# Optimization experiments

Measured on AMD Instinct MI355X. Metric: run time of the kernel, lower is better.

## Reference

```python
import jax, jax.numpy as jnp
import numpy as np

NUM_USERS = 50000
NUM_ITEMS = 10000
NUM_SUPPORT = 5
INPUT_DIM = 512
OUTPUT_DIM = 500
NNZ = 400000


def setup_inputs() -> dict:
    key = jax.random.key(0)
    ks = jax.random.split(key, 6)
    x_u = jax.random.normal(ks[0], (NUM_USERS, INPUT_DIM), dtype=jnp.float32)
    x_v = jax.random.normal(ks[1], (NUM_ITEMS, INPUT_DIM), dtype=jnp.float32)
    # random-uniform-like weight init (weight_variable_random_uniform)
    weights_u = jax.random.normal(ks[2], (INPUT_DIM, OUTPUT_DIM), dtype=jnp.float32) * 0.05
    sup_vals = jax.random.uniform(ks[3], (NUM_SUPPORT, NNZ), dtype=jnp.float32)
    sup_rows = jax.random.randint(ks[4], (NUM_SUPPORT, NNZ), 0, NUM_USERS, dtype=jnp.int32)
    sup_cols = jax.random.randint(ks[5], (NUM_SUPPORT, NNZ), 0, NUM_ITEMS, dtype=jnp.int32)
    return {"x_u": x_u, "x_v": x_v, "weights_u": weights_u,
            "sup_vals": sup_vals, "sup_rows": sup_rows, "sup_cols": sup_cols}


def reference(x_u, x_v, weights_u, sup_vals, sup_rows, sup_cols):
    # share_user_item_weights=True -> weights_v is weights_u; dropout=0.0 -> identity.
    hidden = OUTPUT_DIM // NUM_SUPPORT  # 100
    supports_u, supports_v = [], []
    for i in range(NUM_SUPPORT):
        Wi = jax.lax.dynamic_slice_in_dim(weights_u, i * hidden, hidden, axis=1)
        tmp_u = x_u @ Wi  # [num_users, hidden]
        tmp_v = x_v @ Wi  # [num_items, hidden]
        vals = sup_vals[i][:, None]  # [nnz, 1]
        rows, cols = sup_rows[i], sup_cols[i]
        # support_i @ tmp_v  (sparse [U,I] times dense [I,h])
        su = jax.ops.segment_sum(vals * tmp_v[cols], rows, num_segments=NUM_USERS)
        # support_i^T @ tmp_u (sparse [I,U] times dense [U,h])
        sv = jax.ops.segment_sum(vals * tmp_u[rows], cols, num_segments=NUM_ITEMS)
        supports_u.append(su)
        supports_v.append(sv)
    z_u = jnp.concatenate(supports_u, axis=1)  # [num_users, output_dim]
    z_v = jnp.concatenate(supports_v, axis=1)  # [num_items, output_dim]
    return (jax.nn.relu(z_u), jax.nn.relu(z_v))
```

## Files before the change

### kernel.cpp

```cpp
#include <hip/hip_runtime.h>

#define NUM_USERS   50000
#define NUM_ITEMS   10000
#define NUM_SUPPORT 5
#define INPUT_DIM   512
#define OUTPUT_DIM  500
#define NPAD        512
#define HIDDEN      100
#define HPAD        128
#define NNZ         400000
#define NEDGE       (NUM_SUPPORT * NNZ)

#define CH_E        8192
#define NCHUNK      ((NEDGE + CH_E - 1) / CH_E)
#define NB_U        ((NUM_SUPPORT * NUM_USERS + 255) / 256)
#define NB_V        ((NUM_SUPPORT * NUM_ITEMS + 255) / 256)
#define HISTM_MAX   240000

typedef unsigned int u32;
typedef unsigned short ushort_t;
typedef __attribute__((ext_vector_type(4))) float f32x4;
typedef __attribute__((ext_vector_type(8))) short bf16x8;

#define GLDS(g, l) __builtin_amdgcn_global_load_lds( \
    (const __attribute__((address_space(1))) unsigned int*)(g), \
    (__attribute__((address_space(3))) unsigned int*)(l), 16, 0, 0)

__device__ inline ushort_t bf16_rne(float f) {
    u32 u = __float_as_uint(f);
    u32 r = (u + 0x7FFFu + ((u >> 16) & 1u)) >> 16;
    return (ushort_t)r;
}
__device__ inline float bf16_lo_f32(u32 w) { return __uint_as_float(w << 16); }
__device__ inline float bf16_hi_f32(u32 w) { return __uint_as_float(w & 0xFFFF0000u); }

__global__ __launch_bounds__(256) void cvt_bf16(
    const float4* __restrict__ in, ushort4* __restrict__ out, int n4)
{
    int t = blockIdx.x * 256 + threadIdx.x;
    if (t >= n4) return;
    float4 v = in[t];
    ushort4 o;
    o.x = bf16_rne(v.x); o.y = bf16_rne(v.y);
    o.z = bf16_rne(v.z); o.w = bf16_rne(v.w);
    out[t] = o;
}

__global__ __launch_bounds__(256) void make_WbT(
    const float* __restrict__ W, ushort_t* __restrict__ WbT)
{
    int t = blockIdx.x * 256 + threadIdx.x;
    int n = t >> 9, k = t & 511;
    float v = (n < OUTPUT_DIM) ? W[k * OUTPUT_DIM + n] : 0.f;
    WbT[t] = bf16_rne(v);
}

#define BM 128
#define BN 128
#define BK 32

__global__ __launch_bounds__(256) void gemm_mfma_bf16(
    const ushort_t* __restrict__ A,
    const ushort_t* __restrict__ BT,
    ushort_t* __restrict__ Xp,
    int M)
{
    const int K = INPUT_DIM;
    __shared__ ushort_t As[BM * BK];
    __shared__ ushort_t Bs[BN * BK];

    const int tid  = threadIdx.x;
    const int wave = tid >> 6;
    const int lane = tid & 63;
    const int quad = lane >> 4;
    const int lr   = lane & 15;
    const int m0 = blockIdx.x * BM;
    const int n0 = blockIdx.y * BN;
    const int wm = (wave >> 1) * 64;
    const int wn = (wave & 1) * 64;

    f32x4 acc[4][4] = {};

    for (int k0 = 0; k0 < K; k0 += BK) {
        #pragma unroll
        for (int h = 0; h < 2; ++h) {
            int o   = tid * 16 + h * 4096;
            int row = o >> 6;
            int byt = o & 63;
            int gr  = m0 + row; if (gr >= M) gr = M - 1;
            GLDS((const char*)A + ((long long)gr * K + k0) * 2 + byt, (char*)As + o);
        }
        #pragma unroll
        for (int h = 0; h < 2; ++h) {
            int o   = tid * 16 + h * 4096;
            int row = o >> 6;
            int byt = o & 63;
            GLDS((const char*)BT + ((long long)(n0 + row) * K + k0) * 2 + byt, (char*)Bs + o);
        }
        asm volatile("s_waitcnt vmcnt(0)" ::: "memory");
        __syncthreads();

        bf16x8 af[4], bfr[4];
        #pragma unroll
        for (int tm = 0; tm < 4; ++tm)
            af[tm] = *(const bf16x8*)(As + (wm + tm * 16 + lr) * BK + quad * 8);
        #pragma unroll
        for (int tn = 0; tn < 4; ++tn)
            bfr[tn] = *(const bf16x8*)(Bs + (wn + tn * 16 + lr) * BK + quad * 8);
        #pragma unroll
        for (int tm = 0; tm < 4; ++tm)
            #pragma unroll
            for (int tn = 0; tn < 4; ++tn)
                acc[tm][tn] = __builtin_amdgcn_mfma_f32_16x16x32_bf16(
                    af[tm], bfr[tn], acc[tm][tn], 0, 0, 0);
        __syncthreads();
    }

    #pragma unroll
    for (int tm = 0; tm < 4; ++tm) {
        int rbase = m0 + wm + tm * 16 + quad * 4;
        #pragma unroll
        for (int tn = 0; tn < 4; ++tn) {
            int col = n0 + wn + tn * 16 + lr;
            if (col >= OUTPUT_DIM) continue;
            int seg = col / HIDDEN;
            int off = col - seg * HIDDEN;
            ushort_t* dst = Xp + (long long)seg * M * HPAD + off;
            #pragma unroll
            for (int g = 0; g < 4; ++g) {
                int row = rbase + g;
                if (row < M) dst[(long long)row * HPAD] = bf16_rne(acc[tm][tn][g]);
            }
        }
    }
}

__global__ __launch_bounds__(256) void scan1(u32* __restrict__ data, int n,
                                             u32* __restrict__ partials)
{
    __shared__ u32 sh[256];
    int t = threadIdx.x;
    int base = blockIdx.x * 1024 + t * 4;
    u32 x[4];
    #pragma unroll
    for (int k = 0; k < 4; ++k) {
        int idx = base + k;
        x[k] = (idx < n) ? data[idx] : 0u;
    }
    u32 tsum = x[0] + x[1] + x[2] + x[3];
    sh[t] = tsum;
    __syncthreads();
    for (int off = 1; off < 256; off <<= 1) {
        u32 v = (t >= off) ? sh[t - off] : 0u;
        __syncthreads();
        sh[t] += v;
        __syncthreads();
    }
    u32 run = (t > 0) ? sh[t - 1] : 0u;
    if (t == 255) partials[blockIdx.x] = sh[255];
    #pragma unroll
    for (int k = 0; k < 4; ++k) {
        int idx = base + k;
        if (idx < n) data[idx] = run;
        run += x[k];
    }
}

__global__ __launch_bounds__(256) void scan_partials(u32* __restrict__ partials, int n)
{
    __shared__ u32 sh[256];
    int t = threadIdx.x;
    u32 x = (t < n) ? partials[t] : 0u;
    sh[t] = x;
    __syncthreads();
    for (int off = 1; off < 256; off <<= 1) {
        u32 v = (t >= off) ? sh[t - off] : 0u;
        __syncthreads();
        sh[t] += v;
        __syncthreads();
    }
    if (t < n) partials[t] = (t > 0) ? sh[t - 1] : 0u;
}

__global__ __launch_bounds__(256) void scan_add(u32* __restrict__ data, int n,
                                                const u32* __restrict__ partials)
{
    int idx = blockIdx.x * 256 + threadIdx.x;
    if (idx < n) data[idx] += partials[idx >> 10];
}

template<int NROWS>
__global__ __launch_bounds__(256) void chunk_hist(
    const int* __restrict__ keyidx, u32* __restrict__ histm)
{
    constexpr int NKEY = NUM_SUPPORT * NROWS;
    constexpr int NB = (NKEY + 255) / 256;
    __shared__ u32 hist[NB];
    const int tid = threadIdx.x;
    const int c = blockIdx.x;
    for (int b = tid; b < NB; b += 256) hist[b] = 0u;
    __syncthreads();
    int base = c * CH_E;
    int end = base + CH_E; if (end > NEDGE) end = NEDGE;
    for (int e = base + tid; e < end; e += 256) {
        unsigned i = (unsigned)e / (unsigned)NNZ;
        u32 key = i * (u32)NROWS + (u32)keyidx[e];
        atomicAdd(&hist[key >> 8], 1u);
    }
    __syncthreads();
    for (int b = tid; b < NB; b += 256) histm[b * NCHUNK + c] = hist[b];
}

template<int NROWS, int GSHIFT>
__global__ __launch_bounds__(256) void partition_edges(
    const int* __restrict__ keyidx, const int* __restrict__ gidx,
    const float* __restrict__ vals,
    const u32* __restrict__ histm, uint2* __restrict__ buf)
{
    constexpr int NKEY = NUM_SUPPORT * NROWS;
    constexpr int NB = (NKEY + 255) / 256;
    __shared__ u32 cur[NB];
    const int tid = threadIdx.x;
    const int c = blockIdx.x;
    for (int b = tid; b < NB; b += 256) cur[b] = histm[b * NCHUNK + c];
    __syncthreads();
    int base = c * CH_E;
    int end = base + CH_E; if (end > NEDGE) end = NEDGE;
    for (int e = base + tid; e < end; e += 256) {
        unsigned i = (unsigned)e / (unsigned)NNZ;
        u32 key = i * (u32)NROWS + (u32)keyidx[e];
        u32 p = atomicAdd(&cur[key >> 8], 1u);
        uint2 pay;
        pay.x = __float_as_uint(vals[e]);
        pay.y = (key << GSHIFT) | (u32)gidx[e];
        buf[p] = pay;
    }
}

template<int NROWS, int GSHIFT>
__global__ __launch_bounds__(256) void bucket_scatter(
    const uint2* __restrict__ buf, const u32* __restrict__ histm,
    u32* __restrict__ ptr, uint2* __restrict__ perm)
{
    constexpr int NKEY = NUM_SUPPORT * NROWS;
    constexpr int NB = (NKEY + 255) / 256;
    __shared__ u32 cnt[256];
    __shared__ u32 scn[256];
    const int tid = threadIdx.x;
    const int b = blockIdx.x;
    const u32 key0 = (u32)b << 8;
    const u32 start = histm[b * NCHUNK];
    const u32 bend  = (b + 1 < NB) ? histm[(b + 1) * NCHUNK] : (u32)NEDGE;
    cnt[tid] = 0u;
    __syncthreads();
    for (u32 j = start + tid; j < bend; j += 256) {
        u32 key = buf[j].y >> GSHIFT;
        atomicAdd(&cnt[key - key0], 1u);
    }
    __syncthreads();
    scn[tid] = cnt[tid];
    __syncthreads();
    for (int off = 1; off < 256; off <<= 1) {
        u32 v = (tid >= off) ? scn[tid - off] : 0u;
        __syncthreads();
        scn[tid] += v;
        __syncthreads();
    }
    u32 myoff = start + scn[tid] - cnt[tid];
    if (key0 + (u32)tid < (u32)NKEY) ptr[key0 + tid] = myoff;
    __syncthreads();
    cnt[tid] = myoff;
    __syncthreads();
    for (u32 j = start + tid; j < bend; j += 256) {
        uint2 q = buf[j];
        u32 key = q.y >> GSHIFT;
        u32 p = atomicAdd(&cnt[key - key0], 1u);
        uint2 out;
        out.x = q.x;
        out.y = q.y & ((1u << GSHIFT) - 1u);
        perm[p] = out;
    }
}

__global__ void set_sentinels(u32* __restrict__ a, u32* __restrict__ b)
{
    a[0] = (u32)NEDGE;
    b[0] = (u32)NEDGE;
}

template<int NROWS>
__global__ __launch_bounds__(256) void spmm_pack(
    const u32* __restrict__ ptr,
    const uint2* __restrict__ perm,
    const ushort_t* __restrict__ Xp,
    float* __restrict__ Z,
    int nsrc)
{
    int wv = (int)((blockIdx.x * 256u + threadIdx.x) >> 6);
    wv = __builtin_amdgcn_readfirstlane(wv);
    int lane = threadIdx.x & 63;
    if (wv >= NUM_SUPPORT * NROWS) return;
    int i = wv / NROWS;
    int r = wv - i * NROWS;
    const int g  = lane >> 4;
    const int sl = lane & 15;

    const ushort_t* Xs = Xp + (long long)i * nsrc * HPAD + sl * 8;

    u32 s = ptr[wv], e = ptr[wv + 1];
    float a0 = 0.f, a1 = 0.f, a2 = 0.f, a3 = 0.f;
    float a4 = 0.f, a5 = 0.f, a6 = 0.f, a7 = 0.f;
    u32 k = s + g;
    for (; k + 4 < e; k += 8) {
        uint2 q0 = perm[k], q1 = perm[k + 4];
        float v0 = __uint_as_float(q0.x), v1 = __uint_as_float(q1.x);
        uint4 w0 = *(const uint4*)(Xs + ((long long)q0.y << 7));
        uint4 w1 = *(const uint4*)(Xs + ((long long)q1.y << 7));
        a0 += v0 * bf16_lo_f32(w0.x) + v1 * bf16_lo_f32(w1.x);
        a1 += v0 * bf16_hi_f32(w0.x) + v1 * bf16_hi_f32(w1.x);
        a2 += v0 * bf16_lo_f32(w0.y) + v1 * bf16_lo_f32(w1.y);
        a3 += v0 * bf16_hi_f32(w0.y) + v1 * bf16_hi_f32(w1.y);
        a4 += v0 * bf16_lo_f32(w0.z) + v1 * bf16_lo_f32(w1.z);
        a5 += v0 * bf16_hi_f32(w0.z) + v1 * bf16_hi_f32(w1.z);
        a6 += v0 * bf16_lo_f32(w0.w) + v1 * bf16_lo_f32(w1.w);
        a7 += v0 * bf16_hi_f32(w0.w) + v1 * bf16_hi_f32(w1.w);
    }
    if (k < e) {
        uint2 q0 = perm[k];
        float v0 = __uint_as_float(q0.x);
        uint4 w0 = *(const uint4*)(Xs + ((long long)q0.y << 7));
        a0 += v0 * bf16_lo_f32(w0.x);
        a1 += v0 * bf16_hi_f32(w0.x);
        a2 += v0 * bf16_lo_f32(w0.y);
        a3 += v0 * bf16_hi_f32(w0.y);
        a4 += v0 * bf16_lo_f32(w0.z);
        a5 += v0 * bf16_hi_f32(w0.z);
        a6 += v0 * bf16_lo_f32(w0.w);
        a7 += v0 * bf16_hi_f32(w0.w);
    }
    a0 += __shfl_xor(a0, 16); a0 += __shfl_xor(a0, 32);
    a1 += __shfl_xor(a1, 16); a1 += __shfl_xor(a1, 32);
    a2 += __shfl_xor(a2, 16); a2 += __shfl_xor(a2, 32);
    a3 += __shfl_xor(a3, 16); a3 += __shfl_xor(a3, 32);
    a4 += __shfl_xor(a4, 16); a4 += __shfl_xor(a4, 32);
    a5 += __shfl_xor(a5, 16); a5 += __shfl_xor(a5, 32);
    a6 += __shfl_xor(a6, 16); a6 += __shfl_xor(a6, 32);
    a7 += __shfl_xor(a7, 16); a7 += __shfl_xor(a7, 32);

    if (lane < 13) {
        float* zp = Z + (long long)r * OUTPUT_DIM + i * HIDDEN + lane * 8;
        float4 o0, o1;
        o0.x = a0 > 0.f ? a0 : 0.f;
        o0.y = a1 > 0.f ? a1 : 0.f;
        o0.z = a2 > 0.f ? a2 : 0.f;
        o0.w = a3 > 0.f ? a3 : 0.f;
        *(float4*)zp = o0;
        if (lane < 12) {
            o1.x = a4 > 0.f ? a4 : 0.f;
            o1.y = a5 > 0.f ? a5 : 0.f;
            o1.z = a6 > 0.f ? a6 : 0.f;
            o1.w = a7 > 0.f ? a7 : 0.f;
            *(float4*)(zp + 4) = o1;
        }
    }
}

#define TM 64
#define TN 64
#define TK 16

__global__ __launch_bounds__(256) void gemm_f32(
    const float* __restrict__ A, const float* __restrict__ B,
    float* __restrict__ C, int M, int N, int K, int ldc)
{
    __shared__ float Asl[TK][TM + 4];
    __shared__ float Bsl[TK][TN + 4];
    const int tid = threadIdx.x;
    const int tx  = tid & 15;
    const int ty  = tid >> 4;
    const int row0 = blockIdx.x * TM;
    const int col0 = blockIdx.y * TN;
    float acc[4][4] = {};
    for (int k0 = 0; k0 < K; k0 += TK) {
        #pragma unroll
        for (int it = 0; it < (TM * TK) / 256; ++it) {
            int idx = tid + it * 256;
            int m = idx >> 4, kk = idx & 15, gr = row0 + m;
            Asl[kk][m] = (gr < M) ? A[(long long)gr * K + (k0 + kk)] : 0.f;
        }
        #pragma unroll
        for (int it = 0; it < (TK * TN) / 256; ++it) {
            int idx = tid + it * 256;
            int kk = idx >> 6, n = idx & 63, gc = col0 + n;
            Bsl[kk][n] = (gc < N) ? B[(long long)(k0 + kk) * N + gc] : 0.f;
        }
        __syncthreads();
        #pragma unroll
        for (int kk = 0; kk < TK; ++kk) {
            float a[4], b[4];
            #pragma unroll
            for (int u = 0; u < 4; ++u) a[u] = Asl[kk][ty * 4 + u];
            #pragma unroll
            for (int v = 0; v < 4; ++v) b[v] = Bsl[kk][tx * 4 + v];
            #pragma unroll
            for (int u = 0; u < 4; ++u)
                #pragma unroll
                for (int v = 0; v < 4; ++v)
                    acc[u][v] += a[u] * b[v];
        }
        __syncthreads();
    }
    #pragma unroll
    for (int u = 0; u < 4; ++u) {
        int gr = row0 + ty * 4 + u;
        if (gr >= M) continue;
        #pragma unroll
        for (int v = 0; v < 4; ++v) {
            int gc = col0 + tx * 4 + v;
            if (gc < N) C[(long long)gr * ldc + gc] = acc[u][v];
        }
    }
}

__global__ __launch_bounds__(256) void scatter_edges(
    const float* __restrict__ sup_vals,
    const int*   __restrict__ sup_rows,
    const int*   __restrict__ sup_cols,
    const float* __restrict__ XU, const float* __restrict__ XV,
    float* __restrict__ z_u, float* __restrict__ z_v)
{
    const unsigned t = blockIdx.x * 256u + threadIdx.x;
    const unsigned total = (unsigned)NEDGE * HIDDEN;
    if (t >= total) return;
    const unsigned j  = t % HIDDEN;
    const unsigned eg = t / HIDDEN;
    const unsigned i  = eg / NNZ;
    const float val = sup_vals[eg];
    const int   r   = sup_rows[eg];
    const int   c   = sup_cols[eg];
    const int   colOff = i * HIDDEN + j;
    atomicAdd(&z_u[(long long)r * OUTPUT_DIM + colOff],
              val * XV[(long long)c * NPAD + colOff]);
    atomicAdd(&z_v[(long long)c * OUTPUT_DIM + colOff],
              val * XU[(long long)r * NPAD + colOff]);
}

__global__ __launch_bounds__(256) void relu_inplace(float4* __restrict__ p, int n4)
{
    int t = blockIdx.x * 256 + threadIdx.x;
    if (t >= n4) return;
    float4 v = p[t];
    v.x = v.x > 0.f ? v.x : 0.f;
    v.y = v.y > 0.f ? v.y : 0.f;
    v.z = v.z > 0.f ? v.z : 0.f;
    v.w = v.w > 0.f ? v.w : 0.f;
    p[t] = v;
}

extern "C" void kernel_launch(void* const* d_in, const int* in_sizes, int n_in,
                              void* d_out, int out_size, void* d_ws, size_t ws_size,
                              hipStream_t stream)
{
    const float* x_u      = (const float*)d_in[0];
    const float* x_v      = (const float*)d_in[1];
    const float* W        = (const float*)d_in[2];
    const float* sup_vals = (const float*)d_in[3];
    const int*   sup_rows = (const int*)d_in[4];
    const int*   sup_cols = (const int*)d_in[5];

    float* z_u = (float*)d_out;
    float* z_v = z_u + (long long)NUM_USERS * OUTPUT_DIM;

    const long long NU = (long long)NUM_USERS * 512;
    const long long NV = (long long)NUM_ITEMS * 512;
    const long long PU = (long long)NUM_SUPPORT * NUM_USERS * HPAD;
    const long long PV = (long long)NUM_SUPPORT * NUM_ITEMS * HPAD;
    const int NRU = NUM_SUPPORT * NUM_USERS;
    const int NRV = NUM_SUPPORT * NUM_ITEMS;

    ushort_t* Xp_u  = (ushort_t*)d_ws;
    ushort_t* Xp_v  = Xp_u + PU;
    ushort_t* xu_in = Xp_v + PV;
    ushort_t* xv_in = xu_in + NU;
    ushort_t* WbT   = xv_in + NV;
    u32* row_ptr_u  = (u32*)(WbT + 512 * 512);
    u32* col_ptr_v  = row_ptr_u + (NRU + 1);
    u32* partials   = col_ptr_v + (NRV + 1);
    size_t need_full = ((char*)(partials + 1024)) - ((char*)d_ws);

    uint2* buf    = (uint2*)xu_in;
    u32*   histm  = (u32*)(buf + NEDGE);
    uint2* perm_u = (uint2*)(histm + HISTM_MAX);
    uint2* perm_v = perm_u + NEDGE;

    dim3 blk(256);

    if (ws_size >= need_full) {
        cvt_bf16<<<(int)((NU / 4 + 255) / 256), blk, 0, stream>>>(
            (const float4*)x_u, (ushort4*)xu_in, (int)(NU / 4));
        cvt_bf16<<<(int)((NV / 4 + 255) / 256), blk, 0, stream>>>(
            (const float4*)x_v, (ushort4*)xv_in, (int)(NV / 4));
        make_WbT<<<(512 * 512) / 256, blk, 0, stream>>>(W, WbT);
        gemm_mfma_bf16<<<dim3((NUM_USERS + BM - 1) / BM, 512 / BN), blk, 0, stream>>>(
            xu_in, WbT, Xp_u, NUM_USERS);
        gemm_mfma_bf16<<<dim3((NUM_ITEMS + BM - 1) / BM, 512 / BN), blk, 0, stream>>>(
            xv_in, WbT, Xp_v, NUM_ITEMS);

        auto scan_u32 = [&](u32* data, int n) {
            int nb = (n + 1023) / 1024;
            scan1<<<nb, blk, 0, stream>>>(data, n, partials);
            scan_partials<<<1, blk, 0, stream>>>(partials, nb);
            scan_add<<<(n + 255) / 256, blk, 0, stream>>>(data, n, partials);
        };

        chunk_hist<NUM_USERS><<<NCHUNK, blk, 0, stream>>>(sup_rows, histm);
        scan_u32(histm, NB_U * NCHUNK);
        partition_edges<NUM_USERS, 14><<<NCHUNK, blk, 0, stream>>>(
            sup_rows, sup_cols, sup_vals, histm, buf);
        bucket_scatter<NUM_USERS, 14><<<NB_U, blk, 0, stream>>>(
            buf, histm, row_ptr_u, perm_u);

        chunk_hist<NUM_ITEMS><<<NCHUNK, blk, 0, stream>>>(sup_cols, histm);
        scan_u32(histm, NB_V * NCHUNK);
        partition_edges<NUM_ITEMS, 16><<<NCHUNK, blk, 0, stream>>>(
            sup_cols, sup_rows, sup_vals, histm, buf);
        bucket_scatter<NUM_ITEMS, 16><<<NB_V, blk, 0, stream>>>(
            buf, histm, col_ptr_v, perm_v);

        set_sentinels<<<1, 1, 0, stream>>>(row_ptr_u + NRU, col_ptr_v + NRV);

        spmm_pack<NUM_USERS><<<(NRU * 64 + 255) / 256, blk, 0, stream>>>(
            row_ptr_u, perm_u, Xp_v, z_u, NUM_ITEMS);
        spmm_pack<NUM_ITEMS><<<(NRV * 64 + 255) / 256, blk, 0, stream>>>(
            col_ptr_v, perm_v, Xp_u, z_v, NUM_USERS);
    } else {
        float* XU = (float*)d_ws;
        float* XV = XU + (long long)NUM_USERS * NPAD;
        gemm_f32<<<dim3((NUM_USERS + TM - 1) / TM, (OUTPUT_DIM + TN - 1) / TN),
                   blk, 0, stream>>>(x_u, W, XU, NUM_USERS, OUTPUT_DIM, INPUT_DIM, NPAD);
        gemm_f32<<<dim3((NUM_ITEMS + TM - 1) / TM, (OUTPUT_DIM + TN - 1) / TN),
                   blk, 0, stream>>>(x_v, W, XV, NUM_ITEMS, OUTPUT_DIM, INPUT_DIM, NPAD);
        hipMemsetAsync(d_out, 0, (size_t)out_size * sizeof(float), stream);
        unsigned total = (unsigned)NEDGE * HIDDEN;
        scatter_edges<<<(total + 255u) / 256u, blk, 0, stream>>>(
            sup_vals, sup_rows, sup_cols, XU, XV, z_u, z_v);
        int n4 = out_size / 4;
        relu_inplace<<<(n4 + 255) / 256, blk, 0, stream>>>((float4*)d_out, n4);
    }
}
```

Measured before the change: 581.2 us.

## Pack four output rows per wavefront in SpMM and fuse histogram passes

```diff
diff --git a/kernel.cpp b/kernel.cpp
--- a/kernel.cpp
+++ b/kernel.cpp
@@ -15,7 +15,9 @@
 #define NCHUNK      ((NEDGE + CH_E - 1) / CH_E)
 #define NB_U        ((NUM_SUPPORT * NUM_USERS + 255) / 256)
 #define NB_V        ((NUM_SUPPORT * NUM_ITEMS + 255) / 256)
-#define HISTM_MAX   240000
+#define HISTM_U_SZ  (NB_U * NCHUNK)
+#define HISTM_U_PAD 239366
+#define HISTM_V_SZ  (NB_V * NCHUNK)
 
 typedef unsigned int u32;
 typedef unsigned short ushort_t;
@@ -189,26 +191,29 @@
     if (idx < n) data[idx] += partials[idx >> 10];
 }
 
-template<int NROWS>
-__global__ __launch_bounds__(256) void chunk_hist(
-    const int* __restrict__ keyidx, u32* __restrict__ histm)
-{
-    constexpr int NKEY = NUM_SUPPORT * NROWS;
-    constexpr int NB = (NKEY + 255) / 256;
-    __shared__ u32 hist[NB];
+__global__ __launch_bounds__(256) void hist_uv(
+    const int* __restrict__ rows, const int* __restrict__ cols,
+    u32* __restrict__ histm_u, u32* __restrict__ histm_v)
+{
+    __shared__ u32 hu[NB_U];
+    __shared__ u32 hv[NB_V];
     const int tid = threadIdx.x;
     const int c = blockIdx.x;
-    for (int b = tid; b < NB; b += 256) hist[b] = 0u;
+    for (int b = tid; b < NB_U; b += 256) hu[b] = 0u;
+    for (int b = tid; b < NB_V; b += 256) hv[b] = 0u;
     __syncthreads();
     int base = c * CH_E;
     int end = base + CH_E; if (end > NEDGE) end = NEDGE;
     for (int e = base + tid; e < end; e += 256) {
         unsigned i = (unsigned)e / (unsigned)NNZ;
-        u32 key = i * (u32)NROWS + (u32)keyidx[e];
-        atomicAdd(&hist[key >> 8], 1u);
-    }
-    __syncthreads();
-    for (int b = tid; b < NB; b += 256) histm[b * NCHUNK + c] = hist[b];
+        u32 ku = i * (u32)NUM_USERS + (u32)rows[e];
+        u32 kv = i * (u32)NUM_ITEMS + (u32)cols[e];
+        atomicAdd(&hu[ku >> 8], 1u);
+        atomicAdd(&hv[kv >> 8], 1u);
+    }
+    __syncthreads();
+    for (int b = tid; b < NB_U; b += 256) histm_u[b * NCHUNK + c] = hu[b];
+    for (int b = tid; b < NB_V; b += 256) histm_v[b * NCHUNK + c] = hv[b];
 }
 
 template<int NROWS, int GSHIFT>
@@ -251,6 +256,7 @@
     const u32 key0 = (u32)b << 8;
     const u32 start = histm[b * NCHUNK];
     const u32 bend  = (b + 1 < NB) ? histm[(b + 1) * NCHUNK] : (u32)NEDGE;
+    if (b == 0 && tid == 0) ptr[NKEY] = (u32)NEDGE;
     cnt[tid] = 0u;
     __syncthreads();
     for (u32 j = start + tid; j < bend; j += 256) {
@@ -282,38 +288,48 @@
     }
 }
 
-__global__ void set_sentinels(u32* __restrict__ a, u32* __restrict__ b)
-{
-    a[0] = (u32)NEDGE;
-    b[0] = (u32)NEDGE;
-}
-
 template<int NROWS>
-__global__ __launch_bounds__(256) void spmm_pack(
+__global__ __launch_bounds__(256) void spmm_pack4(
     const u32* __restrict__ ptr,
     const uint2* __restrict__ perm,
     const ushort_t* __restrict__ Xp,
     float* __restrict__ Z,
     int nsrc)
 {
-    int wv = (int)((blockIdx.x * 256u + threadIdx.x) >> 6);
-    wv = __builtin_amdgcn_readfirstlane(wv);
-    int lane = threadIdx.x & 63;
-    if (wv >= NUM_SUPPORT * NROWS) return;
-    int i = wv / NROWS;
-    int r = wv - i * NROWS;
+    constexpr int NKEY = NUM_SUPPORT * NROWS;
+    int w = (int)((blockIdx.x * 256u + threadIdx.x) >> 6);
+    w = __builtin_amdgcn_readfirstlane(w);
+    if (w * 4 >= NKEY) return;
+    const int lane = threadIdx.x & 63;
     const int g  = lane >> 4;
     const int sl = lane & 15;
 
+    int key = w * 4 + g;
+    bool live = key < NKEY;
+    int kc = live ? key : (NKEY - 1);
+    int i = kc / NROWS;
+    int r = kc - i * NROWS;
+    u32 s = ptr[kc];
+    u32 e = live ? ptr[kc + 1] : s;
+
     const ushort_t* Xs = Xp + (long long)i * nsrc * HPAD + sl * 8;
 
-    u32 s = ptr[wv], e = ptr[wv + 1];
+    u32 cnt = e - s;
+    u32 m = cnt;
+    { u32 t = (u32)__shfl_xor((int)m, 16); m = m > t ? m : t; }
+    { u32 t = (u32)__shfl_xor((int)m, 32); m = m > t ? m : t; }
+    int iters = (int)((m + 1) >> 1);
+
     float a0 = 0.f, a1 = 0.f, a2 = 0.f, a3 = 0.f;
     float a4 = 0.f, a5 = 0.f, a6 = 0.f, a7 = 0.f;
-    u32 k = s + g;
-    for (; k + 4 < e; k += 8) {
-        uint2 q0 = perm[k], q1 = perm[k + 4];
-        float v0 = __uint_as_float(q0.x), v1 = __uint_as_float(q1.x);
+    u32 k = s;
+    for (int it = 0; it < iters; ++it) {
+        bool p0 = k < e, p1 = (k + 1) < e;
+        u32 j0 = p0 ? k : 0u;
+        u32 j1 = p1 ? (k + 1) : 0u;
+        uint2 q0 = perm[j0], q1 = perm[j1];
+        float v0 = p0 ? __uint_as_float(q0.x) : 0.f;
+        float v1 = p1 ? __uint_as_float(q1.x) : 0.f;
         uint4 w0 = *(const uint4*)(Xs + ((long long)q0.y << 7));
         uint4 w1 = *(const uint4*)(Xs + ((long long)q1.y << 7));
         a0 += v0 * bf16_lo_f32(w0.x) + v1 * bf16_lo_f32(w1.x);
@@ -324,38 +340,19 @@
         a5 += v0 * bf16_hi_f32(w0.z) + v1 * bf16_hi_f32(w1.z);
         a6 += v0 * bf16_lo_f32(w0.w) + v1 * bf16_lo_f32(w1.w);
         a7 += v0 * bf16_hi_f32(w0.w) + v1 * bf16_hi_f32(w1.w);
-    }
-    if (k < e) {
-        uint2 q0 = perm[k];
-        float v0 = __uint_as_float(q0.x);
-        uint4 w0 = *(const uint4*)(Xs + ((long long)q0.y << 7));
-        a0 += v0 * bf16_lo_f32(w0.x);
-        a1 += v0 * bf16_hi_f32(w0.x);
-        a2 += v0 * bf16_lo_f32(w0.y);
-        a3 += v0 * bf16_hi_f32(w0.y);
-        a4 += v0 * bf16_lo_f32(w0.z);
-        a5 += v0 * bf16_hi_f32(w0.z);
-        a6 += v0 * bf16_lo_f32(w0.w);
-        a7 += v0 * bf16_hi_f32(w0.w);
-    }
-    a0 += __shfl_xor(a0, 16); a0 += __shfl_xor(a0, 32);
-    a1 += __shfl_xor(a1, 16); a1 += __shfl_xor(a1, 32);
-    a2 += __shfl_xor(a2, 16); a2 += __shfl_xor(a2, 32);
-    a3 += __shfl_xor(a3, 16); a3 += __shfl_xor(a3, 32);
-    a4 += __shfl_xor(a4, 16); a4 += __shfl_xor(a4, 32);
-    a5 += __shfl_xor(a5, 16); a5 += __shfl_xor(a5, 32);
-    a6 += __shfl_xor(a6, 16); a6 += __shfl_xor(a6, 32);
-    a7 += __shfl_xor(a7, 16); a7 += __shfl_xor(a7, 32);
-
-    if (lane < 13) {
-        float* zp = Z + (long long)r * OUTPUT_DIM + i * HIDDEN + lane * 8;
-        float4 o0, o1;
+        k += 2;
+    }
+
+    if (live && sl < 13) {
+        float* zp = Z + (long long)r * OUTPUT_DIM + i * HIDDEN + sl * 8;
+        float4 o0;
         o0.x = a0 > 0.f ? a0 : 0.f;
         o0.y = a1 > 0.f ? a1 : 0.f;
         o0.z = a2 > 0.f ? a2 : 0.f;
         o0.w = a3 > 0.f ? a3 : 0.f;
         *(float4*)zp = o0;
-        if (lane < 12) {
+        if (sl < 12) {
+            float4 o1;
             o1.x = a4 > 0.f ? a4 : 0.f;
             o1.y = a5 > 0.f ? a5 : 0.f;
             o1.z = a6 > 0.f ? a6 : 0.f;
@@ -488,10 +485,11 @@
     u32* partials   = col_ptr_v + (NRV + 1);
     size_t need_full = ((char*)(partials + 1024)) - ((char*)d_ws);
 
-    uint2* buf    = (uint2*)xu_in;
-    u32*   histm  = (u32*)(buf + NEDGE);
-    uint2* perm_u = (uint2*)(histm + HISTM_MAX);
-    uint2* perm_v = perm_u + NEDGE;
+    uint2* buf      = (uint2*)xu_in;
+    u32*   histm_u  = (u32*)(buf + NEDGE);
+    u32*   histm_v  = histm_u + HISTM_U_PAD;
+    uint2* perm_u   = (uint2*)(histm_v + HISTM_V_SZ);
+    uint2* perm_v   = perm_u + NEDGE;
 
     dim3 blk(256);
 
@@ -513,25 +511,23 @@
             scan_add<<<(n + 255) / 256, blk, 0, stream>>>(data, n, partials);
         };
 
-        chunk_hist<NUM_USERS><<<NCHUNK, blk, 0, stream>>>(sup_rows, histm);
-        scan_u32(histm, NB_U * NCHUNK);
+        hist_uv<<<NCHUNK, blk, 0, stream>>>(sup_rows, sup_cols, histm_u, histm_v);
+
+        scan_u32(histm_u, HISTM_U_SZ);
         partition_edges<NUM_USERS, 14><<<NCHUNK, blk, 0, stream>>>(
-            sup_rows, sup_cols, sup_vals, histm, buf);
+            sup_rows, sup_cols, sup_vals, histm_u, buf);
         bucket_scatter<NUM_USERS, 14><<<NB_U, blk, 0, stream>>>(
-            buf, histm, row_ptr_u, perm_u);
-
-        chunk_hist<NUM_ITEMS><<<NCHUNK, blk, 0, stream>>>(sup_cols, histm);
-        scan_u32(histm, NB_V * NCHUNK);
+            buf, histm_u, row_ptr_u, perm_u);
+
+        scan_u32(histm_v, HISTM_V_SZ);
         partition_edges<NUM_ITEMS, 16><<<NCHUNK, blk, 0, stream>>>(
-            sup_cols, sup_rows, sup_vals, histm, buf);
+            sup_cols, sup_rows, sup_vals, histm_v, buf);
         bucket_scatter<NUM_ITEMS, 16><<<NB_V, blk, 0, stream>>>(
-            buf, histm, col_ptr_v, perm_v);
-
-        set_sentinels<<<1, 1, 0, stream>>>(row_ptr_u + NRU, col_ptr_v + NRV);
-
-        spmm_pack<NUM_USERS><<<(NRU * 64 + 255) / 256, blk, 0, stream>>>(
+            buf, histm_v, col_ptr_v, perm_v);
+
+        spmm_pack4<NUM_USERS><<<((NRU / 4) * 64) / 256, blk, 0, stream>>>(
             row_ptr_u, perm_u, Xp_v, z_u, NUM_ITEMS);
-        spmm_pack<NUM_ITEMS><<<(NRV * 64 + 255) / 256, blk, 0, stream>>>(
+        spmm_pack4<NUM_ITEMS><<<((NRV / 4) * 64) / 256, blk, 0, stream>>>(
             col_ptr_v, perm_v, Xp_u, z_v, NUM_USERS);
     } else {
         float* XU = (float*)d_ws;
```

After: 568.3 us. -2.2%, faster.
